# Kernel optimization log

Measured on AMD Instinct MI355X. Metric: run time of the kernel, lower is better.

## Reference

```python
import jax, jax.numpy as jnp
import numpy as np

B, S, D, NL, H, KV, F, V, R = 4, 1024, 2048, 2, 16, 4, 8192, 32000, 16
HD = D // H                      # 128, Llama-3 head dim
LORA_SCALE = 32.0 / 16.0         # alpha / r
ROPE_THETA = 500000.0
EPS = 1e-5


def _rope_tables(seq_len, hd):
    inv = 1.0 / (ROPE_THETA ** (jnp.arange(0, hd, 2, dtype=jnp.float32) / hd))
    freqs = jnp.arange(seq_len, dtype=jnp.float32)[:, None] * inv[None, :]   # [S, hd/2]
    emb = jnp.concatenate([freqs, freqs], axis=-1)                           # [S, hd]
    return jnp.cos(emb), jnp.sin(emb)


def _apply_rope(x, cos, sin):
    # x: [B, S, nh, HD]; LLaMA rotate_half convention
    h = x.shape[-1] // 2
    rot = jnp.concatenate([-x[..., h:], x[..., :h]], axis=-1)
    return x * cos[None, :, None, :] + rot * sin[None, :, None, :]


def _rmsnorm(x, w):
    return x * jax.lax.rsqrt(jnp.mean(x * x, axis=-1, keepdims=True) + EPS) * w


def _forward(embed, wq, wk, wv, wo, laq, lbq, lav, lbv, wg, wu, wd, n1, n2, nf,
             input_ids, attention_mask):
    b, s = input_ids.shape
    cos, sin = _rope_tables(s, HD)
    amask = attention_mask.astype(bool)
    # causal AND key-padding mask: [B, 1, S, S]
    mask = jnp.tril(jnp.ones((s, s), bool))[None, None] & amask[:, None, None, :]
    x = embed[input_ids]                                   # [B, S, D]
    for l in range(NL):
        h = _rmsnorm(x, n1[l])
        # base projection + LoRA adapter (q and v only, as in target_modules)
        q = h @ wq[l] + ((h @ laq[l].T) @ lbq[l].T) * LORA_SCALE
        k = h @ wk[l]
        v = h @ wv[l] + ((h @ lav[l].T) @ lbv[l].T) * LORA_SCALE
        q = _apply_rope(q.reshape(b, s, H, HD), cos, sin)
        k = _apply_rope(k.reshape(b, s, KV, HD), cos, sin)
        v = v.reshape(b, s, KV, HD)
        k = jnp.repeat(k, H // KV, axis=2)                 # GQA expand
        v = jnp.repeat(v, H // KV, axis=2)
        scores = jnp.einsum('bqhd,bkhd->bhqk', q, k) / jnp.float32(np.sqrt(HD))
        scores = jnp.where(mask, scores, jnp.float32(-1e9))
        attn = jax.nn.softmax(scores, axis=-1)
        o = jnp.einsum('bhqk,bkhd->bqhd', attn, v).reshape(b, s, D)
        x = x + o @ wo[l]
        h2 = _rmsnorm(x, n2[l])
        x = x + (jax.nn.silu(h2 @ wg[l]) * (h2 @ wu[l])) @ wd[l]
    h = _rmsnorm(x, nf)                                    # final norm -> last_hidden_state
    m = attention_mask.astype(jnp.float32)[..., None]
    return (h * m).sum(axis=1) / jnp.clip(m.sum(axis=1), 1e-9)   # masked mean pool [B, D]


def setup_inputs() -> dict:
    key = jax.random.key(0)
    ks = jax.random.split(key, 14)
    sd = 0.02
    nrm = lambda k, shape: sd * jax.random.normal(k, shape, dtype=jnp.float32)
    return {
        'embed': nrm(ks[0], (V, D)),
        'wq': nrm(ks[1], (NL, D, D)),
        'wk': nrm(ks[2], (NL, D, KV * HD)),
        'wv': nrm(ks[3], (NL, D, KV * HD)),
        'wo': nrm(ks[4], (NL, D, D)),
        'laq': nrm(ks[5], (NL, R, D)),
        'lbq': nrm(ks[6], (NL, D, R)),
        'lav': nrm(ks[7], (NL, R, D)),
        'lbv': nrm(ks[8], (NL, KV * HD, R)),
        'wg': nrm(ks[9], (NL, D, F)),
        'wu': nrm(ks[10], (NL, D, F)),
        'wd': nrm(ks[11], (NL, F, D)),
        'n1': jnp.ones((NL, D), jnp.float32),
        'n2': jnp.ones((NL, D), jnp.float32),
        'nf': jnp.ones((D,), jnp.float32),
        'input_ids': jax.random.randint(ks[12], (B, S), 0, V, dtype=jnp.int32),
        'attention_mask': jnp.ones((B, S), jnp.int32),
    }


def reference(embed, wq, wk, wv, wo, laq, lbq, lav, lbv, wg, wu, wd, n1, n2, nf,
              input_ids, attention_mask):
    return _forward(embed, wq, wk, wv, wo, laq, lbq, lav, lbv, wg, wu, wd,
                    n1, n2, nf, input_ids, attention_mask)
```

## Files before the change

### kernel.cpp

```cpp
#include <hip/hip_runtime.h>
#include <math.h>

#define B_  4
#define S_  1024
#define D_  2048
#define NL_ 2
#define H_  16
#define KV_ 4
#define F_  8192
#define R_  16
#define HD_ 128
#define BS_ (B_*S_)
#define QT2 32
#define KBLK 64

typedef unsigned short u16;
typedef __attribute__((ext_vector_type(8))) __bf16 bf16x8;
typedef __attribute__((ext_vector_type(4))) float  f32x4;

__device__ __forceinline__ u16 f2bf(float f) {
    unsigned x = __float_as_uint(f);
    unsigned r = (x + 0x7fffu + ((x >> 16) & 1u)) >> 16;
    return (u16)r;
}
__device__ __forceinline__ float bf2f(u16 u) {
    return __uint_as_float(((unsigned)u) << 16);
}

__device__ __forceinline__ void gload16(const void* g, void* l) {
    __builtin_amdgcn_global_load_lds((const __attribute__((address_space(1))) void*)g,
                                     (__attribute__((address_space(3))) void*)l, 16, 0, 0);
}

__global__ void embed_kernel(const float* __restrict__ embed,
                             const int* __restrict__ ids,
                             float* __restrict__ x) {
    int tok = blockIdx.x;
    int id  = ids[tok];
    const float4* src = (const float4*)(embed + (size_t)id * D_);
    float4*       dst = (float4*)(x + (size_t)tok * D_);
    for (int i = threadIdx.x; i < D_/4; i += blockDim.x) dst[i] = src[i];
}

template<int OUTBF>
__global__ __launch_bounds__(256) void rmsnorm_kernel(const float* __restrict__ x,
                                                      const float* __restrict__ w,
                                                      void* __restrict__ out) {
    int row = blockIdx.x;
    const float4* xr = (const float4*)(x + (size_t)row * D_);
    float ss = 0.f;
    for (int i = threadIdx.x; i < D_/4; i += 256) {
        float4 v = xr[i];
        ss += v.x*v.x + v.y*v.y + v.z*v.z + v.w*v.w;
    }
    __shared__ float red[4];
    for (int off = 32; off; off >>= 1) ss += __shfl_down(ss, off);
    if ((threadIdx.x & 63) == 0) red[threadIdx.x >> 6] = ss;
    __syncthreads();
    float tot = red[0] + red[1] + red[2] + red[3];
    float scale = rsqrtf(tot / (float)D_ + 1e-5f);
    const float4* w4 = (const float4*)w;
    for (int i = threadIdx.x; i < D_/4; i += 256) {
        float4 v = xr[i], g = w4[i];
        float a = v.x*scale*g.x, b = v.y*scale*g.y, c = v.z*scale*g.z, d = v.w*scale*g.w;
        if (OUTBF) {
            ushort4 o; o.x = f2bf(a); o.y = f2bf(b); o.z = f2bf(c); o.w = f2bf(d);
            ((ushort4*)((u16*)out + (size_t)row * D_))[i] = o;
        } else {
            float4 o; o.x = a; o.y = b; o.z = c; o.w = d;
            ((float4*)((float*)out + (size_t)row * D_))[i] = o;
        }
    }
}

__global__ __launch_bounds__(256) void convt_kernel(const float* __restrict__ in,
                                                    u16* __restrict__ outT,
                                                    int K, int N) {
    __shared__ float tile[32][33];
    int k0 = blockIdx.y * 32, n0 = blockIdx.x * 32;
    int t = threadIdx.x;
    int r = t >> 3, c4 = (t & 7) * 4;
    float4 v = *(const float4*)(in + (size_t)(k0 + r) * N + n0 + c4);
    tile[r][c4] = v.x; tile[r][c4+1] = v.y; tile[r][c4+2] = v.z; tile[r][c4+3] = v.w;
    __syncthreads();
    int n = t >> 3, kc = (t & 7) * 4;
    ushort4 o;
    o.x = f2bf(tile[kc][n]);   o.y = f2bf(tile[kc+1][n]);
    o.z = f2bf(tile[kc+2][n]); o.w = f2bf(tile[kc+3][n]);
    *(ushort4*)(outT + (size_t)(n0 + n) * K + k0 + kc) = o;
}

template<int SLOT>
__global__ __launch_bounds__(256) void convt_gu(const float* __restrict__ in,
                                                u16* __restrict__ outT,
                                                int K, int N) {
    __shared__ float tile[32][33];
    int k0 = blockIdx.y * 32, n0 = blockIdx.x * 32;
    int t = threadIdx.x;
    int r = t >> 3, c4 = (t & 7) * 4;
    float4 v = *(const float4*)(in + (size_t)(k0 + r) * N + n0 + c4);
    tile[r][c4] = v.x; tile[r][c4+1] = v.y; tile[r][c4+2] = v.z; tile[r][c4+3] = v.w;
    __syncthreads();
    int n = t >> 3, kc = (t & 7) * 4;
    ushort4 o;
    o.x = f2bf(tile[kc][n]);   o.y = f2bf(tile[kc+1][n]);
    o.z = f2bf(tile[kc+2][n]); o.w = f2bf(tile[kc+3][n]);
    int orow = n0 + n;
    int wrow = ((orow >> 7) << 8) + SLOT * 128 + (orow & 127);
    *(ushort4*)(outT + (size_t)wrow * K + k0 + kc) = o;
}

template<int ACC>
__global__ __launch_bounds__(256) void gemm_bt(const u16* __restrict__ A,
                                               const u16* __restrict__ Bt,
                                               float* __restrict__ C,
                                               int N, int K) {
    __shared__ __align__(16) u16 As[128*64];
    __shared__ __align__(16) u16 Bs[128*64];
    int tid = threadIdx.x, lane = tid & 63;
    int wid = tid >> 6, wm = wid >> 1, wn = wid & 1;
    int m0 = blockIdx.y * 128, n0 = blockIdx.x * 128;
    const u16* Ab = A  + (size_t)m0 * K;
    const u16* Bb = Bt + (size_t)n0 * K;
    f32x4 acc[4][4] = {};
    for (int k0 = 0; k0 < K; k0 += 64) {
        #pragma unroll
        for (int qq = 0; qq < 4; qq++) {
            int u = qq * 256 + tid;
            int row = u >> 3, cu = u & 7, scu = cu ^ (row & 7);
            size_t goff = (size_t)row * K + k0 + scu * 8;
            gload16(Ab + goff, (char*)As + u * 16);
            gload16(Bb + goff, (char*)Bs + u * 16);
        }
        __syncthreads();
        #pragma unroll
        for (int kk = 0; kk < 2; kk++) {
            int cu = kk * 4 + (lane >> 4);
            bf16x8 af[4], bfr[4];
            #pragma unroll
            for (int i = 0; i < 4; i++) {
                int ar = wm * 64 + i * 16 + (lane & 15);
                af[i]  = *(const bf16x8*)((const char*)As + (((ar << 3) | (cu ^ (ar & 7))) << 4));
                int br = wn * 64 + i * 16 + (lane & 15);
                bfr[i] = *(const bf16x8*)((const char*)Bs + (((br << 3) | (cu ^ (br & 7))) << 4));
            }
            #pragma unroll
            for (int i = 0; i < 4; i++)
                #pragma unroll
                for (int j = 0; j < 4; j++)
                    acc[i][j] = __builtin_amdgcn_mfma_f32_16x16x32_bf16(af[i], bfr[j], acc[i][j], 0, 0, 0);
        }
        __syncthreads();
    }
    int r0 = (lane >> 4) * 4, c0 = lane & 15;
    #pragma unroll
    for (int i = 0; i < 4; i++)
        #pragma unroll
        for (int j = 0; j < 4; j++) {
            int row = m0 + wm * 64 + i * 16 + r0;
            int col = n0 + wn * 64 + j * 16 + c0;
            float* cp = C + (size_t)row * N + col;
            #pragma unroll
            for (int r = 0; r < 4; r++) {
                if (ACC) cp[(size_t)r * N] += acc[i][j][r];
                else     cp[(size_t)r * N] = acc[i][j][r];
            }
        }
}

__global__ __launch_bounds__(512) void gemm_gateup8(const u16* __restrict__ A,
                                                    const u16* __restrict__ Wt,
                                                    u16* __restrict__ act,
                                                    int Nact, int K) {
    __shared__ __align__(16) u16 lds[2][2][256 * 64];
    int tid = threadIdx.x, lane = tid & 63;
    int w = tid >> 6;
    int wm = w >> 2, wn = w & 3;
    int g = lane >> 4, li = lane & 15;
    int m0 = blockIdx.y * 256, n0 = blockIdx.x * 256;
    const u16* Ab = A  + (size_t)m0 * K;
    const u16* Bb = Wt + (size_t)n0 * K;
    int nt = K >> 6;

    f32x4 acc[8][4] = {};

    #define STAGE8(t)                                                              \
        do {                                                                       \
            int p_ = (t) & 1;                                                      \
            int kb_ = (t) << 6;                                                    \
            _Pragma("unroll")                                                      \
            for (int q_ = 0; q_ < 4; q_++) {                                       \
                int u_ = q_ * 512 + tid;                                           \
                int row_ = u_ >> 3, c_ = u_ & 7;                                   \
                int sc_ = c_ ^ (row_ & 7);                                         \
                gload16(Ab + (size_t)row_ * K + kb_ + sc_ * 8,                     \
                        (char*)&lds[p_][0][0] + u_ * 16);                          \
                gload16(Bb + (size_t)row_ * K + kb_ + sc_ * 8,                     \
                        (char*)&lds[p_][1][0] + u_ * 16);                          \
            }                                                                      \
        } while (0)

    STAGE8(0);
    STAGE8(1);

    for (int t = 0; t < nt; t++) {
        int p = t & 1;
        if (t + 1 < nt) { asm volatile("s_waitcnt vmcnt(8)" ::: "memory"); }
        else            { asm volatile("s_waitcnt vmcnt(0)" ::: "memory"); }
        __builtin_amdgcn_s_barrier();
        __builtin_amdgcn_sched_barrier(0);

        bf16x8 bfr[4][2];
        #pragma unroll
        for (int j = 0; j < 4; j++)
            #pragma unroll
            for (int ks = 0; ks < 2; ks++) {
                int br = wn * 64 + j * 16 + li;
                int cu = ks * 4 + g;
                bfr[j][ks] = *(const bf16x8*)((const char*)&lds[p][1][0] +
                                              (((br << 3) | (cu ^ (br & 7))) << 4));
            }
        #pragma unroll
        for (int q = 0; q < 4; q++) {
            bf16x8 af[2][2];
            #pragma unroll
            for (int i = 0; i < 2; i++)
                #pragma unroll
                for (int ks = 0; ks < 2; ks++) {
                    int ar = wm * 128 + q * 32 + i * 16 + li;
                    int cu = ks * 4 + g;
                    af[i][ks] = *(const bf16x8*)((const char*)&lds[p][0][0] +
                                                 (((ar << 3) | (cu ^ (ar & 7))) << 4));
                }
            __builtin_amdgcn_s_setprio(1);
            #pragma unroll
            for (int i = 0; i < 2; i++)
                #pragma unroll
                for (int j = 0; j < 4; j++)
                    #pragma unroll
                    for (int ks = 0; ks < 2; ks++)
                        acc[q * 2 + i][j] = __builtin_amdgcn_mfma_f32_16x16x32_bf16(
                            af[i][ks], bfr[j][ks], acc[q * 2 + i][j], 0, 0, 0);
            __builtin_amdgcn_s_setprio(0);
        }
        __builtin_amdgcn_s_barrier();
        __builtin_amdgcn_sched_barrier(0);
        if (t + 2 < nt) STAGE8(t + 2);
    }
    #undef STAGE8

    __syncthreads();
    float* X = (float*)&lds[0][0][0];
    if (wn >= 2) {
        float* Rr = X + (size_t)(wm * 2 + (wn - 2)) * 8192;
        #pragma unroll
        for (int i = 0; i < 8; i++)
            #pragma unroll
            for (int j = 0; j < 4; j++)
                #pragma unroll
                for (int r = 0; r < 4; r++) {
                    int row = i * 16 + g * 4 + r;
                    int col = j * 16 + li;
                    Rr[row * 64 + (col ^ (((row >> 2) & 3) << 4))] = acc[i][j][r];
                }
    }
    __syncthreads();
    if (wn < 2) {
        const float* Rr = X + (size_t)(wm * 2 + wn) * 8192;
        int colbase = (n0 >> 1) + wn * 64;
        #pragma unroll
        for (int i = 0; i < 8; i++)
            #pragma unroll
            for (int j = 0; j < 4; j++)
                #pragma unroll
                for (int r = 0; r < 4; r++) {
                    int row = i * 16 + g * 4 + r;
                    int col = j * 16 + li;
                    float gv = acc[i][j][r];
                    float uv = Rr[row * 64 + (col ^ (((row >> 2) & 3) << 4))];
                    float s = gv / (1.f + __expf(-gv));
                    act[(size_t)(m0 + wm * 128 + row) * Nact + colbase + col] = f2bf(s * uv);
                }
    }
}

__global__ __launch_bounds__(256) void lora_a_kernel(const u16* __restrict__ h,
                                                     const float* __restrict__ la,
                                                     float* __restrict__ t16) {
    int r = threadIdx.x >> 4;
    int c = threadIdx.x & 15;
    int row = blockIdx.x * 16 + r;
    const ushort4* hr = (const ushort4*)(h + (size_t)row * D_);
    const float4* lr = (const float4*)(la + (size_t)c * D_);
    float acc = 0.f;
    #pragma unroll 4
    for (int i = 0; i < D_/4; i++) {
        ushort4 a = hr[i]; float4 b = lr[i];
        acc += bf2f(a.x)*b.x + bf2f(a.y)*b.y + bf2f(a.z)*b.z + bf2f(a.w)*b.w;
    }
    t16[(size_t)row * R_ + c] = acc;
}

__global__ __launch_bounds__(256) void lora_b_kernel(const float* __restrict__ t16,
                                                     const float* __restrict__ lb,
                                                     float* __restrict__ out, int N) {
    int row = blockIdx.x;
    __shared__ float ts[R_];
    if (threadIdx.x < R_) ts[threadIdx.x] = t16[(size_t)row * R_ + threadIdx.x];
    __syncthreads();
    for (int d = threadIdx.x; d < N; d += 256) {
        const float4* lbr = (const float4*)(lb + (size_t)d * R_);
        float acc = 0.f;
        #pragma unroll
        for (int r4 = 0; r4 < 4; r4++) {
            float4 v = lbr[r4];
            acc += v.x*ts[r4*4] + v.y*ts[r4*4+1] + v.z*ts[r4*4+2] + v.w*ts[r4*4+3];
        }
        out[(size_t)row * N + d] += 2.0f * acc;
    }
}

__global__ void qconv_rope(const float* __restrict__ q, u16* __restrict__ Qc) {
    int tok = blockIdx.x, h = blockIdx.y, t = threadIdx.x;
    int b = tok >> 10, s = tok & (S_ - 1);
    float inv = __expf(-(float)t * (13.122363377404328f / 64.0f));
    float f = (float)s * inv;
    float c = __cosf(f), si = __sinf(f);
    const float* src = q + ((size_t)tok * H_ + h) * HD_;
    float x0 = src[t], x1 = src[t + 64];
    u16* dst = Qc + (((size_t)(b * H_ + h)) * S_ + s) * HD_;
    dst[t]      = f2bf(x0 * c - x1 * si);
    dst[t + 64] = f2bf(x1 * c + x0 * si);
}

__global__ void kconv_rope(const float* __restrict__ k, u16* __restrict__ Kc) {
    int tok = blockIdx.x, h = blockIdx.y, t = threadIdx.x;
    int b = tok >> 10, s = tok & (S_ - 1);
    float inv = __expf(-(float)t * (13.122363377404328f / 64.0f));
    float f = (float)s * inv;
    float c = __cosf(f), si = __sinf(f);
    const float* src = k + ((size_t)tok * KV_ + h) * HD_;
    float x0 = src[t], x1 = src[t + 64];
    u16* dst = Kc + (((size_t)(b * KV_ + h)) * S_ + s) * HD_;
    dst[t]      = f2bf(x0 * c - x1 * si);
    dst[t + 64] = f2bf(x1 * c + x0 * si);
}

__global__ __launch_bounds__(256) void vconv_t(const float* __restrict__ vb,
                                               u16* __restrict__ Vt) {
    __shared__ float tile[32][33];
    int s0 = blockIdx.x * 32, d0 = blockIdx.y * 32;
    int bk = blockIdx.z;
    int b = bk >> 2, kvh = bk & 3;
    int t = threadIdx.x;
    int r = t >> 3, c4 = (t & 7) * 4;
    float4 v = *(const float4*)(vb + (((size_t)(b * S_ + s0 + r)) * KV_ + kvh) * HD_ + d0 + c4);
    tile[r][c4] = v.x; tile[r][c4+1] = v.y; tile[r][c4+2] = v.z; tile[r][c4+3] = v.w;
    __syncthreads();
    int dr = t >> 3, s4 = (t & 7) * 4;
    ushort4 o;
    o.x = f2bf(tile[s4][dr]);   o.y = f2bf(tile[s4+1][dr]);
    o.z = f2bf(tile[s4+2][dr]); o.w = f2bf(tile[s4+3][dr]);
    *(ushort4*)(Vt + (((size_t)(b * KV_ + kvh)) * HD_ + d0 + dr) * S_ + s0 + s4) = o;
}

__global__ __launch_bounds__(512) void flash_attn(const u16* __restrict__ Qc,
                                                  const u16* __restrict__ Kc,
                                                  const u16* __restrict__ Vt,
                                                  const int* __restrict__ am,
                                                  u16* __restrict__ o) {
    __shared__ __align__(16) u16 Ks[64 * 128];
    __shared__ __align__(16) u16 Vs[128 * 64];
    __shared__ __align__(16) u16 Ps[8][16][72];
    __shared__ int am_s[KBLK];
    int qt = blockIdx.x, kvh = blockIdx.y, b = blockIdx.z;
    int tid = threadIdx.x, lane = tid & 63, w = tid >> 6;
    int g = lane >> 4, li = lane & 15;
    int h = kvh * 4 + (w & 3);
    int qrow0 = qt * QT2 + (w >> 2) * 16;

    bf16x8 qf[4];
    const u16* qb = Qc + (((size_t)(b * H_ + h)) * S_ + qrow0 + li) * HD_;
    #pragma unroll
    for (int dd = 0; dd < 4; dd++) qf[dd] = *(const bf16x8*)(qb + dd * 32 + g * 8);

    float m_r[4], l_r[4];
    f32x4 oacc[8];
    #pragma unroll
    for (int r = 0; r < 4; r++) { m_r[r] = -1e30f; l_r[r] = 0.f; }
    #pragma unroll
    for (int d = 0; d < 8; d++) oacc[d] = (f32x4){0.f, 0.f, 0.f, 0.f};

    const u16* Kg = Kc + ((size_t)(b * KV_ + kvh)) * S_ * HD_;
    const u16* Vg = Vt + ((size_t)(b * KV_ + kvh)) * HD_ * S_;
    int qg0 = qrow0 + g * 4;
    int nkv = (qt * QT2 + QT2 - 1) >> 6;

    for (int kvt = 0; kvt <= nkv; kvt++) {
        int kv0 = kvt * KBLK;
        #pragma unroll
        for (int qq = 0; qq < 2; qq++) {
            int u = qq * 512 + tid;
            int krow = u >> 4, p = u & 15;
            gload16(Kg + (size_t)(kv0 + krow) * HD_ + (p ^ (krow & 7)) * 8, (char*)Ks + u * 16);
            int vrow = u >> 3, pv = u & 7;
            gload16(Vg + (size_t)vrow * S_ + kv0 + (pv ^ (vrow & 7)) * 8, (char*)Vs + u * 16);
        }
        if (tid < KBLK) am_s[tid] = am[b * S_ + kv0 + tid];
        __syncthreads();

        if (kv0 <= qrow0 + 15) {
            float ps[4][4];
            #pragma unroll
            for (int kt = 0; kt < 4; kt++) {
                f32x4 sa = (f32x4){0.f, 0.f, 0.f, 0.f};
                int row = kt * 16 + li;
                #pragma unroll
                for (int dd = 0; dd < 4; dd++) {
                    int c = dd * 4 + g;
                    bf16x8 kf = *(const bf16x8*)((const char*)Ks + ((row * 16 + (c ^ (row & 7))) << 4));
                    sa = __builtin_amdgcn_mfma_f32_16x16x32_bf16(qf[dd], kf, sa, 0, 0, 0);
                }
                int kcol = kv0 + kt * 16 + li;
                int amok = am_s[kt * 16 + li];
                #pragma unroll
                for (int r = 0; r < 4; r++) {
                    float s = sa[r] * 0.08838834764831845f;
                    ps[kt][r] = (amok && kcol <= qg0 + r) ? s : -1e9f;
                }
            }

            float rmax[4], rsum[4], scl[4];
            #pragma unroll
            for (int r = 0; r < 4; r++)
                rmax[r] = fmaxf(fmaxf(ps[0][r], ps[1][r]), fmaxf(ps[2][r], ps[3][r]));
            #pragma unroll
            for (int msk = 1; msk < 16; msk <<= 1)
                #pragma unroll
                for (int r = 0; r < 4; r++) rmax[r] = fmaxf(rmax[r], __shfl_xor(rmax[r], msk));
            #pragma unroll
            for (int r = 0; r < 4; r++) {
                float mn = fmaxf(m_r[r], rmax[r]);
                scl[r] = __expf(m_r[r] - mn);
                m_r[r] = mn;
                rsum[r] = 0.f;
            }
            #pragma unroll
            for (int kt = 0; kt < 4; kt++)
                #pragma unroll
                for (int r = 0; r < 4; r++) {
                    float p = __expf(ps[kt][r] - m_r[r]);
                    ps[kt][r] = p;
                    rsum[r] += p;
                }
            #pragma unroll
            for (int msk = 1; msk < 16; msk <<= 1)
                #pragma unroll
                for (int r = 0; r < 4; r++) rsum[r] += __shfl_xor(rsum[r], msk);
            #pragma unroll
            for (int r = 0; r < 4; r++) l_r[r] = l_r[r] * scl[r] + rsum[r];
            #pragma unroll
            for (int d = 0; d < 8; d++)
                #pragma unroll
                for (int r = 0; r < 4; r++) oacc[d][r] *= scl[r];

            #pragma unroll
            for (int kt = 0; kt < 4; kt++)
                #pragma unroll
                for (int r = 0; r < 4; r++)
                    Ps[w][g * 4 + r][kt * 16 + li] = f2bf(ps[kt][r]);
            bf16x8 pf[2];
            #pragma unroll
            for (int ks = 0; ks < 2; ks++)
                pf[ks] = *(const bf16x8*)&Ps[w][li][ks * 32 + g * 8];

            #pragma unroll
            for (int dblk = 0; dblk < 8; dblk++) {
                int row = dblk * 16 + li;
                #pragma unroll
                for (int ks = 0; ks < 2; ks++) {
                    int c = ks * 4 + g;
                    bf16x8 vf = *(const bf16x8*)((const char*)Vs + ((row * 8 + (c ^ (row & 7))) << 4));
                    oacc[dblk] = __builtin_amdgcn_mfma_f32_16x16x32_bf16(pf[ks], vf, oacc[dblk], 0, 0, 0);
                }
            }
        }
        __syncthreads();
    }

    float invl[4];
    #pragma unroll
    for (int r = 0; r < 4; r++) invl[r] = 1.f / l_r[r];
    #pragma unroll
    for (int dblk = 0; dblk < 8; dblk++)
        #pragma unroll
        for (int r = 0; r < 4; r++) {
            int qrow = qg0 + r;
            o[(((size_t)b * S_ + qrow) * H_ + h) * HD_ + dblk * 16 + li] =
                f2bf(oacc[dblk][r] * invl[r]);
        }
}

__global__ __launch_bounds__(256) void pool_kernel(const float* __restrict__ h,
                                                   const int* __restrict__ am,
                                                   float* __restrict__ out) {
    int b = blockIdx.y;
    int d = blockIdx.x * 256 + threadIdx.x;
    float acc = 0.f, ms = 0.f;
    for (int s = 0; s < S_; s++) {
        float mm = (float)am[b * S_ + s];
        ms  += mm;
        acc += mm * h[((size_t)b * S_ + s) * D_ + d];
    }
    out[(size_t)b * D_ + d] = acc / fmaxf(ms, 1e-9f);
}

extern "C" void kernel_launch(void* const* d_in, const int* in_sizes, int n_in,
                              void* d_out, int out_size, void* d_ws, size_t ws_size,
                              hipStream_t stream) {
    const float* embed = (const float*)d_in[0];
    const float* wq    = (const float*)d_in[1];
    const float* wk    = (const float*)d_in[2];
    const float* wv    = (const float*)d_in[3];
    const float* wo    = (const float*)d_in[4];
    const float* laq   = (const float*)d_in[5];
    const float* lbq   = (const float*)d_in[6];
    const float* lav   = (const float*)d_in[7];
    const float* lbv   = (const float*)d_in[8];
    const float* wg    = (const float*)d_in[9];
    const float* wu    = (const float*)d_in[10];
    const float* wd    = (const float*)d_in[11];
    const float* n1    = (const float*)d_in[12];
    const float* n2    = (const float*)d_in[13];
    const float* nf    = (const float*)d_in[14];
    const int*   ids   = (const int*)d_in[15];
    const int*   am    = (const int*)d_in[16];
    float* out = (float*)d_out;

    char* base = (char*)d_ws;
    float* x   = (float*)base;
    u16*   hbf = (u16*)(base + 33554432);
    u16*   obf = (u16*)(base + 50331648);
    char*  Rg  = base + 67108864;
    float* q   = (float*)Rg;
    float* kb  = (float*)(Rg + 33554432);
    float* vb  = (float*)(Rg + 41943040);
    u16*   act = (u16*)Rg;
    float* hf  = (float*)Rg;
    float* t16 = (float*)(base + 134217728);
    u16*   wT0 = (u16*)(base + 134479872);
    u16*   Qc  = (u16*)(base + 201588736);
    u16*   Kc  = (u16*)(base + 218365952);
    u16*   Vtb = (u16*)(base + 222560256);

    embed_kernel<<<BS_, 256, 0, stream>>>(embed, ids, x);

    for (int l = 0; l < NL_; l++) {
        const float* wql = wq + (size_t)l * D_ * D_;
        const float* wkl = wk + (size_t)l * D_ * (KV_*HD_);
        const float* wvl = wv + (size_t)l * D_ * (KV_*HD_);
        const float* wol = wo + (size_t)l * D_ * D_;
        const float* wgl = wg + (size_t)l * D_ * F_;
        const float* wul = wu + (size_t)l * D_ * F_;
        const float* wdl = wd + (size_t)l * F_ * D_;

        rmsnorm_kernel<1><<<BS_, 256, 0, stream>>>(x, n1 + (size_t)l * D_, hbf);

        convt_kernel<<<dim3(D_/32, D_/32), 256, 0, stream>>>(wql, wT0, D_, D_);
        gemm_bt<0><<<dim3(D_/128, BS_/128), 256, 0, stream>>>(hbf, wT0, q, D_, D_);
        lora_a_kernel<<<BS_/16, 256, 0, stream>>>(hbf, laq + (size_t)l * R_ * D_, t16);
        lora_b_kernel<<<BS_, 256, 0, stream>>>(t16, lbq + (size_t)l * D_ * R_, q, D_);

        convt_kernel<<<dim3((KV_*HD_)/32, D_/32), 256, 0, stream>>>(wkl, wT0, D_, KV_*HD_);
        gemm_bt<0><<<dim3((KV_*HD_)/128, BS_/128), 256, 0, stream>>>(hbf, wT0, kb, KV_*HD_, D_);
        convt_kernel<<<dim3((KV_*HD_)/32, D_/32), 256, 0, stream>>>(wvl, wT0, D_, KV_*HD_);
        gemm_bt<0><<<dim3((KV_*HD_)/128, BS_/128), 256, 0, stream>>>(hbf, wT0, vb, KV_*HD_, D_);
        lora_a_kernel<<<BS_/16, 256, 0, stream>>>(hbf, lav + (size_t)l * R_ * D_, t16);
        lora_b_kernel<<<BS_, 256, 0, stream>>>(t16, lbv + (size_t)l * (KV_*HD_) * R_, vb, KV_*HD_);

        qconv_rope<<<dim3(BS_, H_),  64, 0, stream>>>(q,  Qc);
        kconv_rope<<<dim3(BS_, KV_), 64, 0, stream>>>(kb, Kc);
        vconv_t<<<dim3(S_/32, HD_/32, B_*KV_), 256, 0, stream>>>(vb, Vtb);

        flash_attn<<<dim3(S_/QT2, KV_, B_), 512, 0, stream>>>(Qc, Kc, Vtb, am, obf);

        convt_kernel<<<dim3(D_/32, D_/32), 256, 0, stream>>>(wol, wT0, D_, D_);
        gemm_bt<1><<<dim3(D_/128, BS_/128), 256, 0, stream>>>(obf, wT0, x, D_, D_);

        rmsnorm_kernel<1><<<BS_, 256, 0, stream>>>(x, n2 + (size_t)l * D_, hbf);
        convt_gu<0><<<dim3(F_/32, D_/32), 256, 0, stream>>>(wgl, wT0, D_, F_);
        convt_gu<1><<<dim3(F_/32, D_/32), 256, 0, stream>>>(wul, wT0, D_, F_);
        gemm_gateup8<<<dim3((2*F_)/256, BS_/256), 512, 0, stream>>>(hbf, wT0, act, F_, D_);
        convt_kernel<<<dim3(D_/32, F_/32), 256, 0, stream>>>(wdl, wT0, F_, D_);
        gemm_bt<1><<<dim3(D_/128, BS_/128), 256, 0, stream>>>(act, wT0, x, D_, F_);
    }

    rmsnorm_kernel<0><<<BS_, 256, 0, stream>>>(x, nf, hf);
    pool_kernel<<<dim3(D_/256, B_), 256, 0, stream>>>(hf, am, out);
}
```

Measured before the change: 2.118 ms.

## Restructure gate/up GEMM mainloop into 4-slot half-K ring with interleaved staging

Replaces the double-buffered 64-wide K stage in the gate/up GEMM with a four-slot ring of 32-wide K halves. Each half-tile is consumed in two MFMA phases, and the global-to-LDS loads for later halves are issued between those phases. The aim is to keep more loads in flight and to spread memory traffic between compute bursts rather than issuing it all after a full tile. The cost is more barriers per iteration, a more complex swizzle and a new waitcnt bookkeeping scheme that could be wrong or add stalls.

Measured after the change: 2.124 ms. About the same (+0.3%).

```diff
diff --git a/kernel.cpp b/kernel.cpp
--- a/kernel.cpp
+++ b/kernel.cpp
@@ -172,7 +172,7 @@
                                                     const u16* __restrict__ Wt,
                                                     u16* __restrict__ act,
                                                     int Nact, int K) {
-    __shared__ __align__(16) u16 lds[2][2][256 * 64];
+    __shared__ __align__(16) u16 ring[2][4][8192];
     int tid = threadIdx.x, lane = tid & 63;
     int w = tid >> 6;
     int wm = w >> 2, wn = w & 3;
@@ -184,73 +184,104 @@
 
     f32x4 acc[8][4] = {};
 
-    #define STAGE8(t)                                                              \
-        do {                                                                       \
-            int p_ = (t) & 1;                                                      \
-            int kb_ = (t) << 6;                                                    \
-            _Pragma("unroll")                                                      \
-            for (int q_ = 0; q_ < 4; q_++) {                                       \
-                int u_ = q_ * 512 + tid;                                           \
-                int row_ = u_ >> 3, c_ = u_ & 7;                                   \
-                int sc_ = c_ ^ (row_ & 7);                                         \
-                gload16(Ab + (size_t)row_ * K + kb_ + sc_ * 8,                     \
-                        (char*)&lds[p_][0][0] + u_ * 16);                          \
-                gload16(Bb + (size_t)row_ * K + kb_ + sc_ * 8,                     \
-                        (char*)&lds[p_][1][0] + u_ * 16);                          \
-            }                                                                      \
+    #define STG(s, t_, kh, P)                                                        \
+        do {                                                                         \
+            int u_ = (P) * 512 + tid;                                                \
+            int j_ = u_ >> 3, cc_ = u_ & 7;                                          \
+            int sc_ = cc_ ^ (j_ & 7);                                                \
+            int row_ = 2 * j_ + (sc_ >> 2);                                          \
+            int kc_ = (t_) * 64 + (kh) * 32 + (sc_ & 3) * 8;                         \
+            gload16(Ab + (size_t)row_ * K + kc_, (char*)&ring[0][s][0] + u_ * 16);   \
+            gload16(Bb + (size_t)row_ * K + kc_, (char*)&ring[1][s][0] + u_ * 16);   \
         } while (0)
 
-    STAGE8(0);
-    STAGE8(1);
+    #define FRAG(op, s, r) (*(const bf16x8*)((const char*)&ring[op][s][0] +          \
+        (((((r) >> 1) << 3) | (((((r) & 1) << 2) | g) ^ (((r) >> 1) & 7))) << 4)))
+
+    STG(0, 0, 0, 0); STG(0, 0, 0, 1);
+    STG(1, 0, 1, 0); STG(1, 0, 1, 1);
+    STG(2, 1, 0, 0); STG(2, 1, 0, 1);
 
     for (int t = 0; t < nt; t++) {
-        int p = t & 1;
-        if (t + 1 < nt) { asm volatile("s_waitcnt vmcnt(8)" ::: "memory"); }
-        else            { asm volatile("s_waitcnt vmcnt(0)" ::: "memory"); }
+        int s0  = (2 * t) & 3;
+        int s1  = (2 * t + 1) & 3;
+        int sW0 = (2 * t + 3) & 3;
+        int sW1 = s0;
+        bf16x8 af[4], bfr[4];
+
+        if (t == nt - 1) asm volatile("s_waitcnt vmcnt(4)" ::: "memory");
+        else             asm volatile("s_waitcnt vmcnt(8)" ::: "memory");
         __builtin_amdgcn_s_barrier();
         __builtin_amdgcn_sched_barrier(0);
-
-        bf16x8 bfr[4][2];
-        #pragma unroll
-        for (int j = 0; j < 4; j++)
-            #pragma unroll
-            for (int ks = 0; ks < 2; ks++) {
-                int br = wn * 64 + j * 16 + li;
-                int cu = ks * 4 + g;
-                bfr[j][ks] = *(const bf16x8*)((const char*)&lds[p][1][0] +
-                                              (((br << 3) | (cu ^ (br & 7))) << 4));
-            }
-        #pragma unroll
-        for (int q = 0; q < 4; q++) {
-            bf16x8 af[2][2];
-            #pragma unroll
-            for (int i = 0; i < 2; i++)
-                #pragma unroll
-                for (int ks = 0; ks < 2; ks++) {
-                    int ar = wm * 128 + q * 32 + i * 16 + li;
-                    int cu = ks * 4 + g;
-                    af[i][ks] = *(const bf16x8*)((const char*)&lds[p][0][0] +
-                                                 (((ar << 3) | (cu ^ (ar & 7))) << 4));
-                }
-            __builtin_amdgcn_s_setprio(1);
-            #pragma unroll
-            for (int i = 0; i < 2; i++)
-                #pragma unroll
-                for (int j = 0; j < 4; j++)
-                    #pragma unroll
-                    for (int ks = 0; ks < 2; ks++)
-                        acc[q * 2 + i][j] = __builtin_amdgcn_mfma_f32_16x16x32_bf16(
-                            af[i][ks], bfr[j][ks], acc[q * 2 + i][j], 0, 0, 0);
-            __builtin_amdgcn_s_setprio(0);
-        }
+        #pragma unroll
+        for (int j = 0; j < 4; j++) bfr[j] = FRAG(1, s0, wn * 64 + j * 16 + li);
+        #pragma unroll
+        for (int i = 0; i < 4; i++) af[i] = FRAG(0, s0, wm * 128 + i * 16 + li);
+        if (t + 1 < nt) STG(sW0, t + 1, 1, 0);
+        asm volatile("s_waitcnt lgkmcnt(0)" ::: "memory");
+        __builtin_amdgcn_sched_barrier(0);
+        __builtin_amdgcn_s_setprio(1);
+        #pragma unroll
+        for (int i = 0; i < 4; i++)
+            #pragma unroll
+            for (int j = 0; j < 4; j++)
+                acc[i][j] = __builtin_amdgcn_mfma_f32_16x16x32_bf16(af[i], bfr[j], acc[i][j], 0, 0, 0);
+        __builtin_amdgcn_s_setprio(0);
+
         __builtin_amdgcn_s_barrier();
         __builtin_amdgcn_sched_barrier(0);
-        if (t + 2 < nt) STAGE8(t + 2);
-    }
-    #undef STAGE8
+        #pragma unroll
+        for (int i = 0; i < 4; i++) af[i] = FRAG(0, s0, wm * 128 + 64 + i * 16 + li);
+        if (t + 1 < nt) STG(sW0, t + 1, 1, 1);
+        asm volatile("s_waitcnt lgkmcnt(0)" ::: "memory");
+        __builtin_amdgcn_sched_barrier(0);
+        __builtin_amdgcn_s_setprio(1);
+        #pragma unroll
+        for (int i = 0; i < 4; i++)
+            #pragma unroll
+            for (int j = 0; j < 4; j++)
+                acc[4 + i][j] = __builtin_amdgcn_mfma_f32_16x16x32_bf16(af[i], bfr[j], acc[4 + i][j], 0, 0, 0);
+        __builtin_amdgcn_s_setprio(0);
+
+        if (t == nt - 1) asm volatile("s_waitcnt vmcnt(0)" ::: "memory");
+        else             asm volatile("s_waitcnt vmcnt(8)" ::: "memory");
+        __builtin_amdgcn_s_barrier();
+        __builtin_amdgcn_sched_barrier(0);
+        #pragma unroll
+        for (int j = 0; j < 4; j++) bfr[j] = FRAG(1, s1, wn * 64 + j * 16 + li);
+        #pragma unroll
+        for (int i = 0; i < 4; i++) af[i] = FRAG(0, s1, wm * 128 + i * 16 + li);
+        if (t + 2 < nt) STG(sW1, t + 2, 0, 0);
+        asm volatile("s_waitcnt lgkmcnt(0)" ::: "memory");
+        __builtin_amdgcn_sched_barrier(0);
+        __builtin_amdgcn_s_setprio(1);
+        #pragma unroll
+        for (int i = 0; i < 4; i++)
+            #pragma unroll
+            for (int j = 0; j < 4; j++)
+                acc[i][j] = __builtin_amdgcn_mfma_f32_16x16x32_bf16(af[i], bfr[j], acc[i][j], 0, 0, 0);
+        __builtin_amdgcn_s_setprio(0);
+
+        __builtin_amdgcn_s_barrier();
+        __builtin_amdgcn_sched_barrier(0);
+        #pragma unroll
+        for (int i = 0; i < 4; i++) af[i] = FRAG(0, s1, wm * 128 + 64 + i * 16 + li);
+        if (t + 2 < nt) STG(sW1, t + 2, 0, 1);
+        asm volatile("s_waitcnt lgkmcnt(0)" ::: "memory");
+        __builtin_amdgcn_sched_barrier(0);
+        __builtin_amdgcn_s_setprio(1);
+        #pragma unroll
+        for (int i = 0; i < 4; i++)
+            #pragma unroll
+            for (int j = 0; j < 4; j++)
+                acc[4 + i][j] = __builtin_amdgcn_mfma_f32_16x16x32_bf16(af[i], bfr[j], acc[4 + i][j], 0, 0, 0);
+        __builtin_amdgcn_s_setprio(0);
+    }
+    #undef STG
+    #undef FRAG
 
     __syncthreads();
-    float* X = (float*)&lds[0][0][0];
+    float* X = (float*)&ring[0][0][0];
     if (wn >= 2) {
         float* Rr = X + (size_t)(wm * 2 + (wn - 2)) * 8192;
         #pragma unroll
```
